# Kernel tuning notes

Measured on AMD Instinct MI355X. Metric: run time of the kernel, lower is better.

## Reference

```python
import jax, jax.numpy as jnp
import numpy as np

K = 16  # buckets per block (2**treeDepth)
DEPTH = 4

_BIT_BASE = np.array([
 [-1,-1,0,-1,0,0,0,-1,0,0,0,0,0,0,0],[-1,-1,0,-1,0,0,0,1,0,0,0,0,0,0,0],
 [-1,-1,0,1,0,0,0,0,-1,0,0,0,0,0,0],[-1,-1,0,1,0,0,0,0,1,0,0,0,0,0,0],
 [-1,1,0,0,-1,0,0,0,0,-1,0,0,0,0,0],[-1,1,0,0,-1,0,0,0,0,1,0,0,0,0,0],
 [-1,1,0,0,1,0,0,0,0,0,-1,0,0,0,0],[-1,1,0,0,1,0,0,0,0,0,1,0,0,0,0],
 [1,0,-1,0,0,-1,0,0,0,0,0,-1,0,0,0],[1,0,-1,0,0,-1,0,0,0,0,0,1,0,0,0],
 [1,0,-1,0,0,1,0,0,0,0,0,0,-1,0,0],[1,0,-1,0,0,1,0,0,0,0,0,0,1,0,0],
 [1,0,1,0,0,0,-1,0,0,0,0,0,0,-1,0],[1,0,1,0,0,0,-1,0,0,0,0,0,0,1,0],
 [1,0,1,0,0,0,1,0,0,0,0,0,0,0,-1],[1,0,1,0,0,0,1,0,0,0,0,0,0,0,1]], dtype=np.float32)

def make_tree_des_matrix(C):
    # block-diagonal, but off-blocks are ONES per the original code (init with ones)
    m = np.ones((C * K, C * (K - 1)), dtype=np.float32)
    for c in range(C):
        m[c*K:(c+1)*K, c*(K-1):(c+1)*(K-1)] = _BIT_BASE
    return jnp.asarray(m)

def make_selection_matrix(C):
    base = np.zeros((K - 1, DEPTH), dtype=np.float32)
    base[0, 0] = 1.0
    for i in range(1, K - 1):
        base[i, int(np.log2(i + 1))] = 1.0
    sel = np.zeros((C * (K - 1), C * DEPTH), dtype=np.float32)
    for c in range(C):
        sel[c*(K-1):(c+1)*(K-1), c*DEPTH:(c+1)*DEPTH] = base
    return jnp.asarray(sel)

def setup_inputs() -> dict:
    key = jax.random.key(0)
    k1, k2, k3, k4 = jax.random.split(key, 4)
    N, D, C, M = 32768, 1024, 64, 1024
    inputMatrix = jax.random.normal(k1, (N, D), dtype=jnp.float32)
    dims = jax.random.randint(k2, (C * DEPTH,), 0, D)  # gather indices into input columns
    thresholds = jax.random.normal(k3, (C * (K - 1), 1), dtype=jnp.float32)
    lut = jax.random.normal(k4, (M, C, K), dtype=jnp.float32)
    return {
        "inputMatrix": inputMatrix,
        "dims": dims,
        "thresholds": thresholds,
        "lut": lut,
        "selection_matrix": make_selection_matrix(C),
        "tree_des_mat": make_tree_des_matrix(C),
    }

def reference(inputMatrix, dims, thresholds, lut, selection_matrix, tree_des_mat):
    N = inputMatrix.shape[0]
    M, C, Kb = lut.shape
    chosen = inputMatrix[:, dims]                              # [N, C*4]
    subtracted = selection_matrix @ chosen.T - thresholds      # [C*15, N]
    tanh_h = jnp.tanh(subtracted)
    sign_ste = jnp.sign(subtracted) - jax.lax.stop_gradient(tanh_h) + tanh_h
    tree = (tree_des_mat @ sign_ste).T.reshape(N, C, Kb)       # [N, C, 16]
    soft = jax.nn.softmax(tree, axis=2)
    hard = jax.nn.one_hot(jnp.argmax(soft, axis=2), Kb, dtype=soft.dtype)
    encoded = hard - jax.lax.stop_gradient(soft) + soft        # hard-forward / soft-backward STE
    # einsum('nij,kij->nki').sum(2) == full contraction over (C, K)
    out = jnp.einsum('nck,mck->nm', encoded, lut)              # [N, M]
    return out
```

## Files before the change

kernel.cpp:

```cpp
#include <hip/hip_runtime.h>
#include <stdint.h>

#define N_ROWS 32768
#define D_DIM  1024
#define C_TREES 64
#define K_LEAF 16
#define M_OUT  1024

__global__ __launch_bounds__(256) void k_transpose(const float* __restrict__ lut,
                                                   float* __restrict__ lutT) {
    __shared__ float tile[32][33];
    int bx = blockIdx.x;
    int by = blockIdx.y;
    int tx = threadIdx.x;
    int ty = threadIdx.y;
    int src_col = bx * 32 + tx;
#pragma unroll
    for (int i = 0; i < 4; ++i) {
        int src_row = by * 32 + ty + i * 8;
        tile[ty + i * 8][tx] = lut[(size_t)src_row * 1024 + src_col];
    }
    __syncthreads();
    int dst_col = by * 32 + tx;
#pragma unroll
    for (int i = 0; i < 4; ++i) {
        int dst_row = bx * 32 + ty + i * 8;
        lutT[(size_t)dst_row * 1024 + dst_col] = tile[tx][ty + i * 8];
    }
}

__global__ __launch_bounds__(256) void k_encode(const float* __restrict__ in,
                                                const int* __restrict__ dims,
                                                const float* __restrict__ th,
                                                uint8_t* __restrict__ leaf) {
    __shared__ float rows[8][1028];
    __shared__ float th_s[960];
    __shared__ int   dims_s[256];
    int t = threadIdx.x;
    dims_s[t] = dims[t];
    for (int i = t; i < 960; i += 256) th_s[i] = th[i];
    int n0 = blockIdx.x * 8;
    const float4* in4 = (const float4*)(in + (size_t)n0 * 1024);
#pragma unroll
    for (int i = 0; i < 8; ++i) {
        ((float4*)&rows[i][0])[t] = in4[i * 256 + t];
    }
    __syncthreads();
#pragma unroll
    for (int i = 0; i < 2; ++i) {
        int id = i * 256 + t;
        int c = id >> 3;
        int r = id & 7;
        int node = 0;
        const float* trow = &rows[r][0];
#pragma unroll
        for (int lvl = 0; lvl < 4; ++lvl) {
            float x   = trow[dims_s[c * 4 + lvl]];
            float thv = th_s[c * 15 + node];
            node = 2 * node + 1 + ((x > thv) ? 1 : 0);
        }
        leaf[(size_t)c * N_ROWS + n0 + r] = (uint8_t)(node - 15);
    }
}

__global__ __launch_bounds__(512) void k_accum(const float* __restrict__ lutT,
                                               const uint8_t* __restrict__ leaf,
                                               float* __restrict__ out) {
    __shared__ float4 sl[2][16][32];

    int t     = threadIdx.x;
    int mlane = t & 31;
    int ngrp  = t >> 5;
    int wave  = t >> 6;
    int lane  = t & 63;
    int srow  = 2 * wave + (lane >> 5);
    int schunk = lane & 31;

    int m0 = blockIdx.x * 128;
    int n0 = blockIdx.y * 128;

    const float4* lutT4 = (const float4*)lutT;

    auto stage = [&](int buf, int c) {
        const float4* src = lutT4 + ((size_t)(c * 16 + srow) * 256) + (m0 >> 2) + schunk;
        __builtin_amdgcn_global_load_lds((const __attribute__((address_space(1))) void*)src,
                                         (__attribute__((address_space(3))) void*)&sl[buf][2 * wave][0],
                                         16, 0, 0);
    };

    float4 acc[8];
#pragma unroll
    for (int j = 0; j < 8; ++j) acc[j] = make_float4(0.f, 0.f, 0.f, 0.f);

    const uint8_t* lp = leaf + n0 + ngrp * 8;
    uint64_t lv = *(const uint64_t*)lp;
    stage(0, 0);

#pragma unroll 2
    for (int c = 0; c < 64; ++c) {
        __syncthreads();
        if (c < 63) stage((c + 1) & 1, c + 1);
        uint64_t lv_next = (c < 63) ? *(const uint64_t*)(lp + (size_t)(c + 1) * N_ROWS) : 0ull;
        int buf = c & 1;
#pragma unroll
        for (int j = 0; j < 8; ++j) {
            int k = (int)((lv >> (8 * j)) & 15);
            float4 v = sl[buf][k][mlane];
            acc[j].x += v.x; acc[j].y += v.y; acc[j].z += v.z; acc[j].w += v.w;
        }
        lv = lv_next;
    }

    float4* out4 = (float4*)out;
#pragma unroll
    for (int j = 0; j < 8; ++j) {
        int n = n0 + ngrp * 8 + j;
        out4[(size_t)n * 256 + (m0 >> 2) + mlane] = acc[j];
    }
}

extern "C" void kernel_launch(void* const* d_in, const int* in_sizes, int n_in,
                              void* d_out, int out_size, void* d_ws, size_t ws_size,
                              hipStream_t stream) {
    const float* inputMatrix = (const float*)d_in[0];
    const int*   dims        = (const int*)d_in[1];
    const float* thresholds  = (const float*)d_in[2];
    const float* lut         = (const float*)d_in[3];
    float* out = (float*)d_out;

    float*   lutT = (float*)d_ws;
    uint8_t* leaf = (uint8_t*)d_ws + (size_t)4 * 1024 * 1024;

    k_transpose<<<dim3(32, 32), dim3(32, 8), 0, stream>>>(lut, lutT);
    k_encode<<<N_ROWS / 8, 256, 0, stream>>>(inputMatrix, dims, thresholds, leaf);
    k_accum<<<dim3(M_OUT / 128, N_ROWS / 128), 512, 0, stream>>>(lutT, leaf, out);
}
```

Baseline: 342.8 us.

## Pair trees into 256-entry pre-summed LUT tables to halve gather-accumulate steps

Builds a pairwise-summed table P (one row per combination of leaves from two adjacent trees), so the accumulate kernel does 32 gather-adds per output instead of 64. The encoder now emits one byte holding two 4-bit leaf codes, and the accumulate kernel uses larger tiles (1024 rows, 64 columns) with 32 accumulators per thread and XOR-swizzled LDS indexing. The cost is a 32 MB table to build and a larger LDS staging footprint with higher register pressure. The path is taken only when the workspace is large enough, otherwise it falls back to the old kernels.

```diff
diff --git a/kernel.cpp b/kernel.cpp
--- a/kernel.cpp
+++ b/kernel.cpp
@@ -26,6 +26,130 @@
     for (int i = 0; i < 4; ++i) {
         int dst_row = bx * 32 + ty + i * 8;
         lutT[(size_t)dst_row * 1024 + dst_col] = tile[tx][ty + i * 8];
+    }
+}
+
+__global__ __launch_bounds__(256) void k_build(const float* __restrict__ lutT,
+                                               float4* __restrict__ P4) {
+    int j = blockIdx.x;
+    int p = blockIdx.y;
+    int klo = j & 15;
+    int khi = j >> 4;
+    int t = threadIdx.x;
+    const float4* a = (const float4*)lutT + (size_t)(p * 32 + klo) * 256;
+    const float4* b = (const float4*)lutT + (size_t)(p * 32 + 16 + khi) * 256;
+    float4 va = a[t];
+    float4 vb = b[t];
+    float4 v = make_float4(va.x + vb.x, va.y + vb.y, va.z + vb.z, va.w + vb.w);
+    int gsw = (t & ~15) | ((t & 15) ^ klo);
+    P4[((size_t)(p * 256 + j)) * 256 + gsw] = v;
+}
+
+__global__ __launch_bounds__(256) void k_encode2(const float* __restrict__ in,
+                                                 const int* __restrict__ dims,
+                                                 const float* __restrict__ th,
+                                                 uint8_t* __restrict__ code) {
+    __shared__ float rows[8][1028];
+    __shared__ float th_s[960];
+    __shared__ int   dims_s[256];
+    int t = threadIdx.x;
+    dims_s[t] = dims[t];
+    for (int i = t; i < 960; i += 256) th_s[i] = th[i];
+    int n0 = blockIdx.x * 8;
+    const float4* in4 = (const float4*)(in + (size_t)n0 * 1024);
+#pragma unroll
+    for (int i = 0; i < 8; ++i) {
+        ((float4*)&rows[i][0])[t] = in4[i * 256 + t];
+    }
+    __syncthreads();
+    int p = t >> 3;
+    int r = t & 7;
+    const float* trow = &rows[r][0];
+    int cA = 2 * p, cB = 2 * p + 1;
+
+    float xA[4], xB[4];
+#pragma unroll
+    for (int l = 0; l < 4; ++l) {
+        xA[l] = trow[dims_s[cA * 4 + l]];
+        xB[l] = trow[dims_s[cB * 4 + l]];
+    }
+    const float* tAp = &th_s[cA * 15];
+    const float* tBp = &th_s[cB * 15];
+    unsigned mA = 0, mB = 0;
+#pragma unroll
+    for (int i = 0; i < 15; ++i) {
+        const int d = (i == 0) ? 0 : (i < 3) ? 1 : (i < 7) ? 2 : 3;
+        mA |= ((unsigned)(xA[d] > tAp[i])) << i;
+        mB |= ((unsigned)(xB[d] > tBp[i])) << i;
+    }
+    int nA = 0, nB = 0;
+#pragma unroll
+    for (int l = 0; l < 4; ++l) {
+        nA = 2 * nA + 1 + ((mA >> nA) & 1);
+        nB = 2 * nB + 1 + ((mB >> nB) & 1);
+    }
+    code[(size_t)p * N_ROWS + n0 + r] = (uint8_t)(((nB - 15) << 4) | (nA - 15));
+}
+
+__global__ __launch_bounds__(512, 2) void k_accum2(const float4* __restrict__ P4,
+                                                   const uint8_t* __restrict__ code,
+                                                   float* __restrict__ out) {
+    __shared__ float4 sl[2][4096];
+
+    int t  = threadIdx.x;
+    int mc = t & 15;
+    int ng = t >> 4;
+    int m0 = blockIdx.x * 64;
+    int n0 = blockIdx.y * 1024;
+
+    auto stage = [&](int buf, int p) {
+#pragma unroll
+        for (int it = 0; it < 8; ++it) {
+            int idx = t + it * 512;
+            int row = idx >> 4;
+            int ch  = idx & 15;
+            const float4* src = P4 + ((size_t)(p * 256 + row)) * 256 + (m0 >> 2) + ch;
+            __builtin_amdgcn_global_load_lds((const __attribute__((address_space(1))) void*)src,
+                                             (__attribute__((address_space(3))) void*)(&sl[buf][idx]),
+                                             16, 0, 0);
+        }
+    };
+
+    float4 acc[32];
+#pragma unroll
+    for (int j = 0; j < 32; ++j) acc[j] = make_float4(0.f, 0.f, 0.f, 0.f);
+
+    const uint8_t* cp = code + n0 + ng * 32;
+    uint64_t cd[4];
+#pragma unroll
+    for (int q = 0; q < 4; ++q) cd[q] = ((const uint64_t*)cp)[q];
+    stage(0, 0);
+
+    for (int p = 0; p < 32; ++p) {
+        __syncthreads();
+        if (p < 31) stage((p + 1) & 1, p + 1);
+        uint64_t nx0 = 0, nx1 = 0, nx2 = 0, nx3 = 0;
+        if (p < 31) {
+            const uint64_t* np = (const uint64_t*)(cp + (size_t)(p + 1) * N_ROWS);
+            nx0 = np[0]; nx1 = np[1]; nx2 = np[2]; nx3 = np[3];
+        }
+        int buf = p & 1;
+        const float4* s = &sl[buf][0];
+#pragma unroll
+        for (int j = 0; j < 32; ++j) {
+            int cv = (int)((cd[j >> 3] >> ((j & 7) * 8)) & 0xff);
+            int idx = (cv << 4) | (mc ^ (cv & 15));
+            float4 v = s[idx];
+            acc[j].x += v.x; acc[j].y += v.y; acc[j].z += v.z; acc[j].w += v.w;
+        }
+        cd[0] = nx0; cd[1] = nx1; cd[2] = nx2; cd[3] = nx3;
+    }
+
+    float4* out4 = (float4*)out;
+#pragma unroll
+    for (int j = 0; j < 32; ++j) {
+        int n = n0 + ng * 32 + j;
+        out4[(size_t)n * 256 + (m0 >> 2) + mc] = acc[j];
     }
 }
 
@@ -67,7 +191,6 @@
                                                const uint8_t* __restrict__ leaf,
                                                float* __restrict__ out) {
     __shared__ float4 sl[2][16][32];
-
     int t     = threadIdx.x;
     int mlane = t & 31;
     int ngrp  = t >> 5;
@@ -75,27 +198,21 @@
     int lane  = t & 63;
     int srow  = 2 * wave + (lane >> 5);
     int schunk = lane & 31;
-
     int m0 = blockIdx.x * 128;
     int n0 = blockIdx.y * 128;
-
     const float4* lutT4 = (const float4*)lutT;
-
     auto stage = [&](int buf, int c) {
         const float4* src = lutT4 + ((size_t)(c * 16 + srow) * 256) + (m0 >> 2) + schunk;
         __builtin_amdgcn_global_load_lds((const __attribute__((address_space(1))) void*)src,
                                          (__attribute__((address_space(3))) void*)&sl[buf][2 * wave][0],
                                          16, 0, 0);
     };
-
     float4 acc[8];
 #pragma unroll
     for (int j = 0; j < 8; ++j) acc[j] = make_float4(0.f, 0.f, 0.f, 0.f);
-
     const uint8_t* lp = leaf + n0 + ngrp * 8;
     uint64_t lv = *(const uint64_t*)lp;
     stage(0, 0);
-
 #pragma unroll 2
     for (int c = 0; c < 64; ++c) {
         __syncthreads();
@@ -110,7 +227,6 @@
         }
         lv = lv_next;
     }
-
     float4* out4 = (float4*)out;
 #pragma unroll
     for (int j = 0; j < 8; ++j) {
@@ -128,10 +244,24 @@
     const float* lut         = (const float*)d_in[3];
     float* out = (float*)d_out;
 
-    float*   lutT = (float*)d_ws;
-    uint8_t* leaf = (uint8_t*)d_ws + (size_t)4 * 1024 * 1024;
-
-    k_transpose<<<dim3(32, 32), dim3(32, 8), 0, stream>>>(lut, lutT);
-    k_encode<<<N_ROWS / 8, 256, 0, stream>>>(inputMatrix, dims, thresholds, leaf);
-    k_accum<<<dim3(M_OUT / 128, N_ROWS / 128), 512, 0, stream>>>(lutT, leaf, out);
-}
+    float* lutT = (float*)d_ws;
+
+    const size_t NEED = (size_t)4 * 1024 * 1024
+                      + (size_t)32 * 1024 * 1024
+                      + (size_t)1 * 1024 * 1024;
+
+    if (ws_size >= NEED) {
+        float4*  P4   = (float4*)((char*)d_ws + (size_t)4 * 1024 * 1024);
+        uint8_t* codep = (uint8_t*)d_ws + (size_t)36 * 1024 * 1024;
+
+        k_transpose<<<dim3(32, 32), dim3(32, 8), 0, stream>>>(lut, lutT);
+        k_build<<<dim3(256, 32), 256, 0, stream>>>(lutT, P4);
+        k_encode2<<<N_ROWS / 8, 256, 0, stream>>>(inputMatrix, dims, thresholds, codep);
+        k_accum2<<<dim3(M_OUT / 64, N_ROWS / 1024), 512, 0, stream>>>(P4, codep, out);
+    } else {
+        uint8_t* leaf = (uint8_t*)d_ws + (size_t)4 * 1024 * 1024;
+        k_transpose<<<dim3(32, 32), dim3(32, 8), 0, stream>>>(lut, lutT);
+        k_encode<<<N_ROWS / 8, 256, 0, stream>>>(inputMatrix, dims, thresholds, leaf);
+        k_accum<<<dim3(M_OUT / 128, N_ROWS / 128), 512, 0, stream>>>(lutT, leaf, out);
+    }
+}
```

After: 378.2 us. 1.1x slower.
